# Optimization experiments

Measured on AMD Instinct MI355X. Metric: run time of the kernel, lower is better.

The kernel has to match this reference:

```python
import jax, jax.numpy as jnp
import numpy as np

TOP_K = 4


def setup_inputs() -> dict:
    key = jax.random.key(0)
    ks = jax.random.split(key, 5)
    B, T, D = 2, 1024, 1024
    P, PD = 256, 32  # n_patterns, pattern_dim
    return {
        "x": jax.random.normal(ks[0], (B, T, D), dtype=jnp.float32),
        "hasher_w": jax.random.normal(ks[1], (PD, D), dtype=jnp.float32) * 0.03,
        "keys": jax.random.normal(ks[2], (P, PD), dtype=jnp.float32) * 0.1,
        "values_down": jax.random.normal(ks[3], (P, D, PD), dtype=jnp.float32) * 0.01,
        "values_up": jax.random.normal(ks[4], (P, PD, D), dtype=jnp.float32) * 0.01,
        "scale": jnp.full((1,), 0.1, dtype=jnp.float32),
    }


def reference(x, hasher_w, keys, values_down, values_up, scale):
    # h = hasher(x): [B,T,pattern_dim]
    h = jnp.einsum("btd,pd->btp", x, hasher_w)
    # similarity to pattern keys: [B,T,n_patterns]
    sim = jnp.einsum("btp,np->btn", h, keys)
    vals, idx = jax.lax.top_k(sim, TOP_K)          # [B,T,TOP_K]
    w = jax.nn.softmax(vals, axis=-1)              # softmax over the top-k scores
    out = jnp.zeros_like(x)
    for k in range(TOP_K):  # small fixed loop, matches original
        ik = idx[..., k]                            # [B,T] int32
        vd = values_down[ik]                        # [B,T,D,PD] gathered per-token
        vu = values_up[ik]                          # [B,T,PD,D]
        proj = jax.nn.silu(jnp.einsum("btd,btdp->btp", x, vd))
        o = jnp.einsum("btp,btpd->btd", proj, vu)
        out = out + o * w[..., k:k + 1]
    return x + out * scale
```

## Files before the change

kernel.cpp:

```cpp
#include <hip/hip_runtime.h>
#include <math.h>
#include <float.h>

#define DDIM 1024
#define PDIM 32
#define NPAT 256
#define TOPK 4
#define BLOCK 256
#define GT   16
#define DCHP 128
#define NCHP 8
#define RTPB 4

__global__ __launch_bounds__(BLOCK) void route_kernel(
    const float* __restrict__ x,
    const float* __restrict__ hasher_w,
    const float* __restrict__ keys,
    int*   __restrict__ tki,
    float* __restrict__ tkw,
    int ntok)
{
    __shared__ float P_s[RTPB][64 * 33];
    __shared__ float h_s[RTPB][32];

    const int tid  = threadIdx.x;
    const int wv   = tid >> 6;
    const int lane = tid & 63;
    const int tok  = min(blockIdx.x * RTPB + wv, ntok - 1);

    const float4* xrow = (const float4*)(x + (size_t)tok * DDIM);
    float4 xr[4];
    #pragma unroll
    for (int i = 0; i < 4; ++i) xr[i] = xrow[i * 64 + lane];

    float part[PDIM];
    #pragma unroll
    for (int pp = 0; pp < PDIM; ++pp) {
        const float4* wrow = (const float4*)(hasher_w + (size_t)pp * DDIM);
        float a = 0.f;
        #pragma unroll
        for (int i = 0; i < 4; ++i) {
            const float4 w4 = wrow[i * 64 + lane];
            a = fmaf(xr[i].x, w4.x, a); a = fmaf(xr[i].y, w4.y, a);
            a = fmaf(xr[i].z, w4.z, a); a = fmaf(xr[i].w, w4.w, a);
        }
        part[pp] = a;
    }

    float* P = P_s[wv];
    #pragma unroll
    for (int pp = 0; pp < PDIM; ++pp) P[lane * 33 + pp] = part[pp];
    __syncthreads();

    {
        const int pp = lane & 31, half = lane >> 5;
        float hsum = 0.f;
        #pragma unroll 8
        for (int i = 0; i < 32; ++i)
            hsum += P[(half * 32 + i) * 33 + pp];
        hsum += __shfl_xor(hsum, 32, 64);
        if (half == 0) h_s[wv][pp] = hsum;
    }
    __syncthreads();

    float4 h4[8];
    #pragma unroll
    for (int i = 0; i < 8; ++i) h4[i] = *(const float4*)&h_s[wv][i * 4];

    float sc0, sc1, sc2, sc3;
    {
        float sv[4];
        #pragma unroll
        for (int c = 0; c < 4; ++c) {
            const float4* kr = (const float4*)(keys + (size_t)(c * 64 + lane) * PDIM);
            float a = 0.f;
            #pragma unroll
            for (int i = 0; i < 8; ++i) {
                const float4 k4 = kr[i];
                a = fmaf(k4.x, h4[i].x, a); a = fmaf(k4.y, h4[i].y, a);
                a = fmaf(k4.z, h4[i].z, a); a = fmaf(k4.w, h4[i].w, a);
            }
            sv[c] = a;
        }
        sc0 = sv[0]; sc1 = sv[1]; sc2 = sv[2]; sc3 = sv[3];
    }

    float wval[TOPK]; int widx[TOPK];
    #pragma unroll
    for (int r = 0; r < TOPK; ++r) {
        float bv = sc0; int bc = 0;
        if (sc1 > bv) { bv = sc1; bc = 1; }
        if (sc2 > bv) { bv = sc2; bc = 2; }
        if (sc3 > bv) { bv = sc3; bc = 3; }
        int bidx = bc * 64 + lane;
        #pragma unroll
        for (int off = 1; off < 64; off <<= 1) {
            const float ov = __shfl_xor(bv, off, 64);
            const int   oi = __shfl_xor(bidx, off, 64);
            if (ov > bv || (ov == bv && oi < bidx)) { bv = ov; bidx = oi; }
        }
        wval[r] = bv; widx[r] = bidx;
        if ((bidx & 63) == lane) {
            const int c = bidx >> 6;
            if (c == 0) sc0 = -FLT_MAX;
            else if (c == 1) sc1 = -FLT_MAX;
            else if (c == 2) sc2 = -FLT_MAX;
            else sc3 = -FLT_MAX;
        }
    }

    if (lane == 0) {
        float m = wval[0];
        #pragma unroll
        for (int k = 1; k < TOPK; ++k) m = fmaxf(m, wval[k]);
        float s = 0.f, e[TOPK];
        #pragma unroll
        for (int k = 0; k < TOPK; ++k) { e[k] = expf(wval[k] - m); s += e[k]; }
        #pragma unroll
        for (int k = 0; k < TOPK; ++k) {
            tki[tok * TOPK + k] = widx[k];
            tkw[tok * TOPK + k] = e[k] / s;
        }
    }
}

__global__ __launch_bounds__(NPAT) void scanfill_kernel(
    const int* __restrict__ tki, const float* __restrict__ tkw,
    const float* __restrict__ scale_p,
    int* __restrict__ offs,
    int* __restrict__ etok, float* __restrict__ ew, int* __restrict__ slotof,
    int* __restrict__ tile2p, int* __restrict__ tilei,
    int nent, int maxt)
{
    __shared__ int s[NPAT];
    __shared__ int cur[NPAT];
    const int tid = threadIdx.x;

    cur[tid] = 0;
    __syncthreads();
    for (int e = tid; e < nent; e += NPAT) atomicAdd(&cur[tki[e]], 1);
    __syncthreads();

    const int v = cur[tid];
    s[tid] = v;
    __syncthreads();
    for (int off = 1; off < NPAT; off <<= 1) {
        int t = 0;
        if (tid >= off) t = s[tid - off];
        __syncthreads();
        s[tid] += t;
        __syncthreads();
    }
    const int incl = s[tid];
    offs[tid + 1] = incl;
    if (tid == 0) offs[0] = 0;
    cur[tid] = incl - v;
    __syncthreads();

    const int tc = (v + GT - 1) / GT;
    s[tid] = tc;
    __syncthreads();
    for (int off = 1; off < NPAT; off <<= 1) {
        int t = 0;
        if (tid >= off) t = s[tid - off];
        __syncthreads();
        s[tid] += t;
        __syncthreads();
    }
    const int toff = s[tid] - tc;
    for (int i = tid; i < maxt; i += NPAT) tile2p[i] = -1;
    __syncthreads();
    for (int i = 0; i < tc; ++i) { tile2p[toff + i] = tid; tilei[toff + i] = i; }

    const float sc = scale_p[0];
    for (int e = tid; e < nent; e += NPAT) {
        const int p = tki[e];
        const int slot = atomicAdd(&cur[p], 1);
        etok[slot] = e >> 2;
        ew[slot]   = tkw[e] * sc;
        slotof[e]  = slot;
    }
}

__global__ __launch_bounds__(BLOCK, 6) void proj_kernel(
    const float* __restrict__ x,
    const float* __restrict__ vd,
    const int* __restrict__ offs,
    const int* __restrict__ etok,
    const int* __restrict__ tile2p,
    const int* __restrict__ tilei,
    float* __restrict__ part,
    int nent)
{
    __shared__ float vd_s[DCHP * PDIM];
    __shared__ float x_s[GT * DCHP];
    __shared__ int   gt[GT];
    __shared__ int   gs[GT];

    const int tb  = blockIdx.x >> 3;
    const int c   = blockIdx.x & 7;
    const int p   = tile2p[tb];
    if (p < 0) return;
    const int tid = threadIdx.x;
    const int off0 = offs[p] + tilei[tb] * GT;
    const int gv   = min(GT, offs[p + 1] - off0);

    const float* vdp = vd + (size_t)p * DDIM * PDIM + (size_t)c * DCHP * PDIM;
    #pragma unroll
    for (int k = 0; k < 4; ++k)
        ((float4*)vd_s)[k * 256 + tid] = ((const float4*)vdp)[k * 256 + tid];

    if (tid < GT) {
        if (tid < gv) { gt[tid] = etok[off0 + tid]; gs[tid] = off0 + tid; }
        else          { gt[tid] = etok[off0];       gs[tid] = nent; }
    }
    __syncthreads();

    #pragma unroll
    for (int k = 0; k < 2; ++k) {
        const int q  = k * 256 + tid;
        const int g  = q >> 5, fi = q & 31;
        ((float4*)x_s)[g * 32 + fi] =
            *(const float4*)(x + (size_t)gt[g] * DDIM + c * DCHP + fi * 4);
    }
    __syncthreads();

    const int lane = tid & 63;
    const int wv   = tid >> 6;
    const int pp4  = lane & 7;
    const int seg  = lane >> 3;

    float4 acc[4];
    #pragma unroll
    for (int j = 0; j < 4; ++j) acc[j] = make_float4(0.f, 0.f, 0.f, 0.f);

    #pragma unroll
    for (int i4 = 0; i4 < 4; ++i4) {
        const int d0 = seg * 16 + i4 * 4;
        const float4 v0 = *(const float4*)&vd_s[(d0 + 0) * PDIM + pp4 * 4];
        const float4 v1 = *(const float4*)&vd_s[(d0 + 1) * PDIM + pp4 * 4];
        const float4 v2 = *(const float4*)&vd_s[(d0 + 2) * PDIM + pp4 * 4];
        const float4 v3 = *(const float4*)&vd_s[(d0 + 3) * PDIM + pp4 * 4];
        #pragma unroll
        for (int j = 0; j < 4; ++j) {
            const float4 xg = *(const float4*)&x_s[(wv * 4 + j) * DCHP + d0];
            acc[j].x = fmaf(xg.x, v0.x, acc[j].x);
            acc[j].y = fmaf(xg.x, v0.y, acc[j].y);
            acc[j].z = fmaf(xg.x, v0.z, acc[j].z);
            acc[j].w = fmaf(xg.x, v0.w, acc[j].w);
            acc[j].x = fmaf(xg.y, v1.x, acc[j].x);
            acc[j].y = fmaf(xg.y, v1.y, acc[j].y);
            acc[j].z = fmaf(xg.y, v1.z, acc[j].z);
            acc[j].w = fmaf(xg.y, v1.w, acc[j].w);
            acc[j].x = fmaf(xg.z, v2.x, acc[j].x);
            acc[j].y = fmaf(xg.z, v2.y, acc[j].y);
            acc[j].z = fmaf(xg.z, v2.z, acc[j].z);
            acc[j].w = fmaf(xg.z, v2.w, acc[j].w);
            acc[j].x = fmaf(xg.w, v3.x, acc[j].x);
            acc[j].y = fmaf(xg.w, v3.y, acc[j].y);
            acc[j].z = fmaf(xg.w, v3.z, acc[j].z);
            acc[j].w = fmaf(xg.w, v3.w, acc[j].w);
        }
    }

    #pragma unroll
    for (int j = 0; j < 4; ++j) {
        #pragma unroll
        for (int off = 8; off <= 32; off <<= 1) {
            acc[j].x += __shfl_xor(acc[j].x, off, 64);
            acc[j].y += __shfl_xor(acc[j].y, off, 64);
            acc[j].z += __shfl_xor(acc[j].z, off, 64);
            acc[j].w += __shfl_xor(acc[j].w, off, 64);
        }
    }

    float* partc = part + (size_t)c * (size_t)(nent + 1) * PDIM;
    if ((lane & 0x38) == 0) {
        #pragma unroll
        for (int j = 0; j < 4; ++j)
            *(float4*)&partc[(size_t)gs[wv * 4 + j] * PDIM + pp4 * 4] = acc[j];
    }
}

template <int MODE>
__global__ __launch_bounds__(BLOCK, 6) void up_kernel(
    const float* __restrict__ vu,
    const int* __restrict__ offs,
    const int* __restrict__ etok,
    const float* __restrict__ ew,
    const int* __restrict__ tile2p,
    const int* __restrict__ tilei,
    const float* __restrict__ part,
    float* __restrict__ dst,
    int nent)
{
    __shared__ float vu_s[PDIM * DCHP];
    __shared__ float projT[PDIM][20];
    __shared__ int   gt[GT];
    __shared__ float gw[GT];
    __shared__ int   gs[GT];

    const int tb  = blockIdx.x >> 3;
    const int c   = blockIdx.x & 7;
    const int p   = tile2p[tb];
    if (p < 0) return;
    const int tid = threadIdx.x;
    const int off0 = offs[p] + tilei[tb] * GT;
    const int gv   = min(GT, offs[p + 1] - off0);

    const size_t PS = (size_t)(nent + 1) * PDIM;

    const float* vup = vu + (size_t)p * PDIM * DDIM + (size_t)c * DCHP;
    #pragma unroll
    for (int k = 0; k < 4; ++k) {
        const int q  = k * 256 + tid;
        const int pp = q >> 5, fi = q & 31;
        *(float4*)&vu_s[pp * DCHP + fi * 4] =
            *(const float4*)(vup + (size_t)pp * DDIM + fi * 4);
    }
    if (tid < GT) {
        if (tid < gv) {
            gt[tid] = etok[off0 + tid];
            gw[tid] = ew[off0 + tid];
            gs[tid] = off0 + tid;
        } else {
            gt[tid] = etok[off0]; gw[tid] = 0.f; gs[tid] = nent;
        }
    }
    __syncthreads();

    #pragma unroll
    for (int r = 0; r < 2; ++r) {
        const int idx = tid + r * BLOCK;
        const int g = idx >> 5, pp = idx & 31;
        const size_t row = (size_t)gs[g] * PDIM + pp;
        float s = 0.f;
        #pragma unroll
        for (int i = 0; i < NCHP; ++i) s += part[i * PS + row];
        const float pj = s / (1.f + expf(-s));
        projT[pp][g] = pj * gw[g];
    }
    __syncthreads();

    const int tg  = tid >> 5;
    const int l32 = tid & 31;
    const int g0 = tg * 2, g1 = tg * 2 + 1;

    float4 o0 = make_float4(0.f, 0.f, 0.f, 0.f);
    float4 o1 = o0;
    #pragma unroll
    for (int pp = 0; pp < PDIM; ++pp) {
        const float4 vu4 = *(const float4*)&vu_s[pp * DCHP + l32 * 4];
        const float a = projT[pp][g0];
        const float b = projT[pp][g1];
        o0.x = fmaf(a, vu4.x, o0.x); o0.y = fmaf(a, vu4.y, o0.y);
        o0.z = fmaf(a, vu4.z, o0.z); o0.w = fmaf(a, vu4.w, o0.w);
        o1.x = fmaf(b, vu4.x, o1.x); o1.y = fmaf(b, vu4.y, o1.y);
        o1.z = fmaf(b, vu4.z, o1.z); o1.w = fmaf(b, vu4.w, o1.w);
    }

    if (MODE == 0) {
        *(float4*)(dst + (size_t)gs[g0] * DDIM + c * DCHP + l32 * 4) = o0;
        *(float4*)(dst + (size_t)gs[g1] * DDIM + c * DCHP + l32 * 4) = o1;
    } else {
        if (g0 < gv) {
            float* op = dst + (size_t)gt[g0] * DDIM + c * DCHP + l32 * 4;
            atomicAdd(op + 0, o0.x); atomicAdd(op + 1, o0.y);
            atomicAdd(op + 2, o0.z); atomicAdd(op + 3, o0.w);
        }
        if (g1 < gv) {
            float* op = dst + (size_t)gt[g1] * DDIM + c * DCHP + l32 * 4;
            atomicAdd(op + 0, o1.x); atomicAdd(op + 1, o1.y);
            atomicAdd(op + 2, o1.z); atomicAdd(op + 3, o1.w);
        }
    }
}

__global__ __launch_bounds__(BLOCK) void combine_kernel(
    const float* __restrict__ x, const float* __restrict__ contrib,
    const int* __restrict__ slotof, float* __restrict__ out)
{
    __shared__ int sl[TOPK];
    const int t = blockIdx.x, tid = threadIdx.x;
    if (tid < TOPK) sl[tid] = slotof[t * TOPK + tid];
    __syncthreads();
    float4 r = ((const float4*)(x + (size_t)t * DDIM))[tid];
    #pragma unroll
    for (int k = 0; k < TOPK; ++k) {
        const float4 cv = ((const float4*)(contrib + (size_t)sl[k] * DDIM))[tid];
        r.x += cv.x; r.y += cv.y; r.z += cv.z; r.w += cv.w;
    }
    ((float4*)(out + (size_t)t * DDIM))[tid] = r;
}

extern "C" void kernel_launch(void* const* d_in, const int* in_sizes, int n_in,
                              void* d_out, int out_size, void* d_ws, size_t ws_size,
                              hipStream_t stream) {
    const float* x        = (const float*)d_in[0];
    const float* hasher_w = (const float*)d_in[1];
    const float* keys     = (const float*)d_in[2];
    const float* vd       = (const float*)d_in[3];
    const float* vu       = (const float*)d_in[4];
    const float* scale    = (const float*)d_in[5];
    float* out = (float*)d_out;

    const int ntok = in_sizes[0] / DDIM;
    if (ntok <= 0) return;
    const int nent = ntok * TOPK;
    const int maxt = (nent + GT - 1) / GT + NPAT;

    char* w = (char*)d_ws;
    const size_t o_offs = 1024;
    const size_t o_tki  = 2560;
    const size_t o_tkw  = o_tki  + (size_t)nent * 4;
    const size_t o_etok = o_tkw  + (size_t)nent * 4;
    const size_t o_ew   = o_etok + (size_t)nent * 4;
    const size_t o_slot = o_ew   + (size_t)nent * 4;
    const size_t o_t2p  = o_slot + (size_t)nent * 4;
    const size_t o_tli  = o_t2p  + (size_t)maxt * 4;
    const size_t o_part = (o_tli + (size_t)maxt * 4 + 255) & ~(size_t)255;
    const size_t partsz = (size_t)NCHP * (size_t)(nent + 1) * PDIM * 4;
    const size_t o_ctb  = (o_part + partsz + 255) & ~(size_t)255;
    const size_t needPart    = o_ctb;
    const size_t needContrib = o_ctb + (size_t)(nent + 1) * DDIM * 4;

    int*   offs   = (int*)(w + o_offs);
    int*   tki    = (int*)(w + o_tki);
    float* tkw    = (float*)(w + o_tkw);
    int*   etok   = (int*)(w + o_etok);
    float* ew     = (float*)(w + o_ew);
    int*   slotof = (int*)(w + o_slot);
    int*   tile2p = (int*)(w + o_t2p);
    int*   tilei  = (int*)(w + o_tli);
    float* part   = (float*)(w + o_part);
    float* contrib= (float*)(w + o_ctb);

    const int rblocks = (ntok + RTPB - 1) / RTPB;
    hipLaunchKernelGGL(route_kernel, dim3(rblocks), dim3(BLOCK), 0, stream,
                       x, hasher_w, keys, tki, tkw, ntok);
    hipLaunchKernelGGL(scanfill_kernel, dim3(1), dim3(NPAT), 0, stream,
                       tki, tkw, scale, offs, etok, ew, slotof,
                       tile2p, tilei, nent, maxt);
    hipLaunchKernelGGL(proj_kernel, dim3(maxt * NCHP), dim3(BLOCK), 0, stream,
                       x, vd, offs, etok, tile2p, tilei, part, nent);

    if (ws_size >= needContrib) {
        hipLaunchKernelGGL((up_kernel<0>), dim3(maxt * NCHP), dim3(BLOCK), 0, stream,
                           vu, offs, etok, ew, tile2p, tilei, part, contrib, nent);
        hipLaunchKernelGGL(combine_kernel, dim3(ntok), dim3(BLOCK), 0, stream,
                           x, contrib, slotof, out);
    } else if (ws_size >= needPart) {
        hipMemcpyAsync(out, x, (size_t)ntok * DDIM * 4, hipMemcpyDeviceToDevice,
                       stream);
        hipLaunchKernelGGL((up_kernel<1>), dim3(maxt * NCHP), dim3(BLOCK), 0, stream,
                           vu, offs, etok, ew, tile2p, tilei, part, out, nent);
    }
}
```

Before: 208.9 us.

## Stage hasher weights in LDS and parallelize expert histogram and slot fill

The route kernel now loads hasher_w chunks cooperatively into shared memory and reuses them across the block's four tokens, instead of each wave reading the full weight matrix from global memory. Per-pattern counts are accumulated with global atomics inside the route kernel. The single-block scanfill is split into a small scan kernel and a grid-wide fill kernel, so the serial per-entry loop in one block becomes parallel. This adds a memset, an extra launch and global atomic contention, and slot order becomes nondeterministic.

Result: faster. 186.0 us (-11.0%).

```diff
diff --git a/kernel.cpp b/kernel.cpp
--- a/kernel.cpp
+++ b/kernel.cpp
@@ -18,15 +18,17 @@
     const float* __restrict__ keys,
     int*   __restrict__ tki,
     float* __restrict__ tkw,
+    int*   __restrict__ gcount,
     int ntok)
 {
-    __shared__ float P_s[RTPB][64 * 33];
+    __shared__ float shmem[RTPB * 64 * 33];
     __shared__ float h_s[RTPB][32];
 
     const int tid  = threadIdx.x;
     const int wv   = tid >> 6;
     const int lane = tid & 63;
-    const int tok  = min(blockIdx.x * RTPB + wv, ntok - 1);
+    const int traw = blockIdx.x * RTPB + wv;
+    const int tok  = min(traw, ntok - 1);
 
     const float4* xrow = (const float4*)(x + (size_t)tok * DDIM);
     float4 xr[4];
@@ -35,19 +37,30 @@
 
     float part[PDIM];
     #pragma unroll
-    for (int pp = 0; pp < PDIM; ++pp) {
-        const float4* wrow = (const float4*)(hasher_w + (size_t)pp * DDIM);
-        float a = 0.f;
-        #pragma unroll
-        for (int i = 0; i < 4; ++i) {
-            const float4 w4 = wrow[i * 64 + lane];
-            a = fmaf(xr[i].x, w4.x, a); a = fmaf(xr[i].y, w4.y, a);
-            a = fmaf(xr[i].z, w4.z, a); a = fmaf(xr[i].w, w4.w, a);
-        }
-        part[pp] = a;
-    }
-
-    float* P = P_s[wv];
+    for (int pp = 0; pp < PDIM; ++pp) part[pp] = 0.f;
+
+    float* hs = shmem;
+    for (int i = 0; i < 4; ++i) {
+        #pragma unroll
+        for (int k = 0; k < 8; ++k) {
+            const int q  = k * 256 + tid;
+            const int pp = q >> 6, fi = q & 63;
+            ((float4*)hs)[q] =
+                *(const float4*)(hasher_w + (size_t)pp * DDIM + i * 256 + fi * 4);
+        }
+        __syncthreads();
+        #pragma unroll
+        for (int pp = 0; pp < PDIM; ++pp) {
+            const float4 w4 = *(const float4*)&hs[pp * 256 + lane * 4];
+            part[pp] = fmaf(xr[i].x, w4.x, part[pp]);
+            part[pp] = fmaf(xr[i].y, w4.y, part[pp]);
+            part[pp] = fmaf(xr[i].z, w4.z, part[pp]);
+            part[pp] = fmaf(xr[i].w, w4.w, part[pp]);
+        }
+        __syncthreads();
+    }
+
+    float* P = shmem + wv * (64 * 33);
     #pragma unroll
     for (int pp = 0; pp < PDIM; ++pp) P[lane * 33 + pp] = part[pp];
     __syncthreads();
@@ -109,7 +122,7 @@
         }
     }
 
-    if (lane == 0) {
+    if (lane == 0 && traw < ntok) {
         float m = wval[0];
         #pragma unroll
         for (int k = 1; k < TOPK; ++k) m = fmaxf(m, wval[k]);
@@ -120,28 +133,22 @@
         for (int k = 0; k < TOPK; ++k) {
             tki[tok * TOPK + k] = widx[k];
             tkw[tok * TOPK + k] = e[k] / s;
-        }
-    }
-}
-
-__global__ __launch_bounds__(NPAT) void scanfill_kernel(
-    const int* __restrict__ tki, const float* __restrict__ tkw,
-    const float* __restrict__ scale_p,
+            atomicAdd(&gcount[widx[k]], 1);
+        }
+    }
+}
+
+__global__ __launch_bounds__(NPAT) void scan_kernel(
+    const int* __restrict__ gcount,
     int* __restrict__ offs,
-    int* __restrict__ etok, float* __restrict__ ew, int* __restrict__ slotof,
+    int* __restrict__ gcur,
     int* __restrict__ tile2p, int* __restrict__ tilei,
-    int nent, int maxt)
+    int maxt)
 {
     __shared__ int s[NPAT];
-    __shared__ int cur[NPAT];
     const int tid = threadIdx.x;
 
-    cur[tid] = 0;
-    __syncthreads();
-    for (int e = tid; e < nent; e += NPAT) atomicAdd(&cur[tki[e]], 1);
-    __syncthreads();
-
-    const int v = cur[tid];
+    const int v = gcount[tid];
     s[tid] = v;
     __syncthreads();
     for (int off = 1; off < NPAT; off <<= 1) {
@@ -154,10 +161,10 @@
     const int incl = s[tid];
     offs[tid + 1] = incl;
     if (tid == 0) offs[0] = 0;
-    cur[tid] = incl - v;
-    __syncthreads();
+    gcur[tid] = incl - v;
 
     const int tc = (v + GT - 1) / GT;
+    __syncthreads();
     s[tid] = tc;
     __syncthreads();
     for (int off = 1; off < NPAT; off <<= 1) {
@@ -171,15 +178,22 @@
     for (int i = tid; i < maxt; i += NPAT) tile2p[i] = -1;
     __syncthreads();
     for (int i = 0; i < tc; ++i) { tile2p[toff + i] = tid; tilei[toff + i] = i; }
-
-    const float sc = scale_p[0];
-    for (int e = tid; e < nent; e += NPAT) {
-        const int p = tki[e];
-        const int slot = atomicAdd(&cur[p], 1);
-        etok[slot] = e >> 2;
-        ew[slot]   = tkw[e] * sc;
-        slotof[e]  = slot;
-    }
+}
+
+__global__ __launch_bounds__(BLOCK) void fill_kernel(
+    const int* __restrict__ tki, const float* __restrict__ tkw,
+    const float* __restrict__ scale_p,
+    int* __restrict__ gcur,
+    int* __restrict__ etok, float* __restrict__ ew, int* __restrict__ slotof,
+    int nent)
+{
+    const int e = blockIdx.x * BLOCK + threadIdx.x;
+    if (e >= nent) return;
+    const int p = tki[e];
+    const int slot = atomicAdd(&gcur[p], 1);
+    etok[slot] = e >> 2;
+    ew[slot]   = tkw[e] * scale_p[0];
+    slotof[e]  = slot;
 }
 
 __global__ __launch_bounds__(BLOCK, 6) void proj_kernel(
@@ -410,8 +424,10 @@
     const int maxt = (nent + GT - 1) / GT + NPAT;
 
     char* w = (char*)d_ws;
-    const size_t o_offs = 1024;
-    const size_t o_tki  = 2560;
+    const size_t o_gcnt = 0;
+    const size_t o_gcur = 1024;
+    const size_t o_offs = 2048;
+    const size_t o_tki  = 4096;
     const size_t o_tkw  = o_tki  + (size_t)nent * 4;
     const size_t o_etok = o_tkw  + (size_t)nent * 4;
     const size_t o_ew   = o_etok + (size_t)nent * 4;
@@ -424,6 +440,8 @@
     const size_t needPart    = o_ctb;
     const size_t needContrib = o_ctb + (size_t)(nent + 1) * DDIM * 4;
 
+    int*   gcount = (int*)(w + o_gcnt);
+    int*   gcur   = (int*)(w + o_gcur);
     int*   offs   = (int*)(w + o_offs);
     int*   tki    = (int*)(w + o_tki);
     float* tkw    = (float*)(w + o_tkw);
@@ -435,12 +453,15 @@
     float* part   = (float*)(w + o_part);
     float* contrib= (float*)(w + o_ctb);
 
+    hipMemsetAsync(gcount, 0, NPAT * sizeof(int), stream);
+
     const int rblocks = (ntok + RTPB - 1) / RTPB;
     hipLaunchKernelGGL(route_kernel, dim3(rblocks), dim3(BLOCK), 0, stream,
-                       x, hasher_w, keys, tki, tkw, ntok);
-    hipLaunchKernelGGL(scanfill_kernel, dim3(1), dim3(NPAT), 0, stream,
-                       tki, tkw, scale, offs, etok, ew, slotof,
-                       tile2p, tilei, nent, maxt);
+                       x, hasher_w, keys, tki, tkw, gcount, ntok);
+    hipLaunchKernelGGL(scan_kernel, dim3(1), dim3(NPAT), 0, stream,
+                       gcount, offs, gcur, tile2p, tilei, maxt);
+    hipLaunchKernelGGL(fill_kernel, dim3((nent + BLOCK - 1) / BLOCK), dim3(BLOCK),
+                       0, stream, tki, tkw, scale, gcur, etok, ew, slotof, nent);
     hipLaunchKernelGGL(proj_kernel, dim3(maxt * NCHP), dim3(BLOCK), 0, stream,
                        x, vd, offs, etok, tile2p, tilei, part, nent);
 
```
